# Kernel tuning notes

Hardware: AMD Instinct MI355X
Metric: run time of the kernel (lower is better)

The kernel has to match this reference:

```python
import jax, jax.numpy as jnp
import numpy as np

EPS = 1e-6
NEG = -10000.0
B, T, V, D, H, L, F = 2, 1024, 32000, 1024, 16, 4, 2730
DH = D // H
SCALE = 1.0 / np.sqrt(DH)


def alibi_slopes(n_head):
    # standard ALiBi geometric slopes (n_head is a power of 2 here)
    start = 2.0 ** (-8.0 / n_head)
    return jnp.asarray([start ** (i + 1) for i in range(n_head)], dtype=jnp.float32)


def rational_softmax(x, eps=EPS):
    # exp-free softmax: Pade [0/2] rational surrogate of exp on shifted (<=0) scores
    s = x - jnp.max(x, axis=-1, keepdims=True)
    num = 1.0 / (1.0 - s + 0.5 * s * s)
    return num / (jnp.sum(num, axis=-1, keepdims=True) + eps)


def me_norm(x, w, eps=EPS):
    # mean-error norm: x / (mean|x| + eps) * w
    return x / (jnp.mean(jnp.abs(x), axis=-1, keepdims=True) + eps) * w


def setup_inputs() -> dict:
    key = jax.random.key(0)
    ks = jax.random.split(key, 9)
    std = 0.02
    return {
        "input_ids": jax.random.randint(ks[0], (B, T), 0, V),
        "embed_w":   jax.random.normal(ks[1], (V, D), jnp.float32) * std,  # tied with head
        "qkv_w":     jax.random.normal(ks[2], (L, 3 * D, D), jnp.float32) * std,
        "out_w":     jax.random.normal(ks[3], (L, D, D), jnp.float32) * std,
        "gate_w":    jax.random.normal(ks[4], (L, 2 * F, D), jnp.float32) * std,
        "wout_w":    jax.random.normal(ks[5], (L, D, F), jnp.float32) * std,
        "norm1_w":   jnp.ones((L, D), jnp.float32),
        "norm2_w":   jnp.ones((L, D), jnp.float32),
        "normf_w":   jnp.ones((D,), jnp.float32),
    }


def _forward(input_ids, embed_w, qkv_w, out_w, gate_w, wout_w, norm1_w, norm2_w, normf_w):
    slopes = alibi_slopes(H)                       # [H]
    pos = jnp.arange(T)
    rel = jnp.abs(pos[:, None] - pos[None, :]).astype(jnp.float32)  # [T,T]
    alibi = -rel[None] * slopes[:, None, None]     # [H,T,T]
    causal = jnp.triu(jnp.ones((T, T), bool), k=1) # future positions

    x = embed_w[input_ids]                         # [B,T,D]

    def block(x, p):
        w_qkv, w_out, w_gate, w_wout, n1, n2 = p
        h = me_norm(x, n1)
        qkv = (h @ w_qkv.T).reshape(B, T, 3, H, DH).transpose(2, 0, 3, 1, 4)
        q, k, v = qkv[0], qkv[1], qkv[2]           # [B,H,T,DH]
        scores = jnp.einsum('bhtd,bhsd->bhts', q, k) * SCALE + alibi
        scores = jnp.where(causal[None, None], NEG, scores)
        probs = rational_softmax(scores)
        o = jnp.einsum('bhts,bhsd->bhtd', probs, v)
        o = o.transpose(0, 2, 1, 3).reshape(B, T, D)
        x = x + o @ w_out.T
        h = me_norm(x, n2)
        gv = h @ w_gate.T                           # [B,T,2F]
        gate, val = gv[..., :F], gv[..., F:]
        sigma = 0.5 * (gate / (jnp.abs(gate) + 1.0) + 1.0)  # rational sigmoid
        x = x + (gate * sigma * val) @ w_wout.T
        return x, None

    x, _ = jax.lax.scan(block, x, (qkv_w, out_w, gate_w, wout_w, norm1_w, norm2_w))
    x = me_norm(x, normf_w)
    logits = x @ embed_w.T                          # tied head, [B,T,V]
    return logits


def reference(input_ids, embed_w, qkv_w, out_w, gate_w, wout_w, norm1_w, norm2_w, normf_w):
    return _forward(input_ids, embed_w, qkv_w, out_w, gate_w, wout_w, norm1_w, norm2_w, normf_w)
```

## Files before the change

kernel.cpp:

```cpp
#include <hip/hip_runtime.h>
#include <math.h>

typedef __attribute__((ext_vector_type(8))) short bf16x8;
typedef __attribute__((ext_vector_type(4))) float f32x4;

namespace {
constexpr int Bc = 2, Tc = 1024, Dc = 1024, Hc = 16, Fc = 2730;
constexpr int Fp = 2752;
constexpr int Gp = 5504;
constexpr int Mc = Bc * Tc;
constexpr float EPSc = 1e-6f;
constexpr float NEGc = -10000.0f;
constexpr float SCALEc = 0.125f;
}

__device__ __forceinline__ unsigned short f2b(float f) {
    unsigned int u = __float_as_uint(f);
    u += 0x7FFFu + ((u >> 16) & 1u);
    return (unsigned short)(u >> 16);
}

__global__ void k_embed(const int* __restrict__ ids, const float* __restrict__ ew,
                        float* __restrict__ x) {
    int row = blockIdx.x;
    int id = ids[row];
    const float4* src = (const float4*)(ew + (size_t)id * Dc);
    float4* dst = (float4*)(x + (size_t)row * Dc);
    dst[threadIdx.x] = src[threadIdx.x];
}

__global__ void k_conv(const float* __restrict__ in, unsigned short* __restrict__ out) {
    size_t i = ((size_t)blockIdx.x * 256 + threadIdx.x) * 4;
    float4 v = *(const float4*)(in + i);
    ushort4 o;
    o.x = f2b(v.x); o.y = f2b(v.y); o.z = f2b(v.z); o.w = f2b(v.w);
    *(ushort4*)(out + i) = o;
}

__global__ void k_conv_gate_ilv(const float* __restrict__ in, unsigned short* __restrict__ out) {
    int r = blockIdx.x;
    int c = threadIdx.x * 4;
    ushort4 o;
    if (r < 2 * Fc) {
        int src = (r >> 1) + (r & 1) * Fc;
        float4 v = *(const float4*)(in + (size_t)src * Dc + c);
        o.x = f2b(v.x); o.y = f2b(v.y); o.z = f2b(v.z); o.w = f2b(v.w);
    } else {
        o.x = o.y = o.z = o.w = 0;
    }
    *(ushort4*)(out + (size_t)r * Dc + c) = o;
}

__global__ void k_conv_padk(const float* __restrict__ in, unsigned short* __restrict__ out) {
    int r = blockIdx.x;
    for (int c = threadIdx.x; c < Fp; c += 256) {
        float v = (c < Fc) ? in[(size_t)r * Fc + c] : 0.0f;
        out[(size_t)r * Fp + c] = f2b(v);
    }
}

__global__ void k_menorm_b(const float* __restrict__ x, const float* __restrict__ w,
                           unsigned short* __restrict__ out) {
    int row = blockIdx.x;
    float4 v = ((const float4*)(x + (size_t)row * Dc))[threadIdx.x];
    float s = fabsf(v.x) + fabsf(v.y) + fabsf(v.z) + fabsf(v.w);
#pragma unroll
    for (int m = 32; m >= 1; m >>= 1) s += __shfl_xor(s, m);
    __shared__ float ws4[4];
    if ((threadIdx.x & 63) == 0) ws4[threadIdx.x >> 6] = s;
    __syncthreads();
    float tot = ws4[0] + ws4[1] + ws4[2] + ws4[3];
    float inv = 1.0f / (tot / (float)Dc + EPSc);
    float4 wv = ((const float4*)w)[threadIdx.x];
    ushort4 o;
    o.x = f2b(v.x * inv * wv.x);
    o.y = f2b(v.y * inv * wv.y);
    o.z = f2b(v.z * inv * wv.z);
    o.w = f2b(v.w * inv * wv.w);
    ((ushort4*)(out + (size_t)row * Dc))[threadIdx.x] = o;
}

template <int MODE, int BM>
__global__ __launch_bounds__(256) void k_mfma_gemm(
    const unsigned short* __restrict__ A, const unsigned short* __restrict__ Bw,
    const float* __restrict__ Res, float* __restrict__ C,
    unsigned short* __restrict__ U0, unsigned short* __restrict__ U1,
    unsigned short* __restrict__ U2, int N, int K) {
    constexpr int MFR = BM / 32;
    __shared__ __align__(16) unsigned short As[BM * 64];
    __shared__ __align__(16) unsigned short Bs[128 * 64];
    const int tid = threadIdx.x;
    const int lane = tid & 63;
    const int wid = tid >> 6;
    const int wr = wid >> 1, wc = wid & 1;
    const int l15 = lane & 15, g = lane >> 4;

    const int nwg = gridDim.x * gridDim.y;
    int w = blockIdx.y * gridDim.x + blockIdx.x;
    int f = (nwg & 7) ? w : ((w & 7) * (nwg >> 3) + (w >> 3));
    const int bm = (f % gridDim.x) * BM, bn = (f / gridDim.x) * 128;

    f32x4 acc[MFR][4] = {};

    const int nk = K >> 6;
    for (int kt = 0; kt < nk; ++kt) {
        const int k0 = kt << 6;
#pragma unroll
        for (int it = 0; it < MFR; ++it) {
            int ci = it * 256 + tid;
            int r = ci >> 3;
            int sc = (ci & 7) ^ (r & 7);
            __builtin_amdgcn_global_load_lds(
                (const __attribute__((address_space(1))) void*)(A + (size_t)(bm + r) * K + k0 + sc * 8),
                (__attribute__((address_space(3))) void*)(As + ci * 8), 16, 0, 0);
        }
#pragma unroll
        for (int it = 0; it < 4; ++it) {
            int ci = it * 256 + tid;
            int r = ci >> 3;
            int sc = (ci & 7) ^ (r & 7);
            __builtin_amdgcn_global_load_lds(
                (const __attribute__((address_space(1))) void*)(Bw + (size_t)(bn + r) * K + k0 + sc * 8),
                (__attribute__((address_space(3))) void*)(Bs + ci * 8), 16, 0, 0);
        }
        __syncthreads();
#pragma unroll
        for (int kk = 0; kk < 2; ++kk) {
            bf16x8 af[MFR], bfr[4];
            const int kc = kk * 4 + g;
#pragma unroll
            for (int m = 0; m < MFR; ++m) {
                int row = wr * (BM / 2) + m * 16 + l15;
                af[m] = *(const bf16x8*)&As[(row * 8 + (kc ^ (row & 7))) * 8];
            }
#pragma unroll
            for (int n = 0; n < 4; ++n) {
                int col = wc * 64 + n * 16 + l15;
                bfr[n] = *(const bf16x8*)&Bs[(col * 8 + (kc ^ (col & 7))) * 8];
            }
#pragma unroll
            for (int m = 0; m < MFR; ++m)
#pragma unroll
                for (int n = 0; n < 4; ++n)
                    acc[m][n] = __builtin_amdgcn_mfma_f32_16x16x32_bf16(af[m], bfr[n], acc[m][n], 0, 0, 0);
        }
        __syncthreads();
    }

#pragma unroll
    for (int m = 0; m < MFR; ++m) {
        int row0 = bm + wr * (BM / 2) + m * 16 + (g << 2);
#pragma unroll
        for (int n = 0; n < 4; ++n) {
            int col = bn + wc * 64 + n * 16 + l15;
            if constexpr (MODE == 0 || MODE == 1) {
#pragma unroll
                for (int j = 0; j < 4; ++j) {
                    size_t idx = (size_t)(row0 + j) * N + col;
                    float v = acc[m][n][j];
                    if (MODE == 1) v += Res[idx];
                    C[idx] = v;
                }
            } else if constexpr (MODE == 2) {
                if (col < 2048) {
                    unsigned short* dst = (col < 1024) ? U0 : U1;
                    int hh = (col & 1023) >> 6, dh = col & 63;
#pragma unroll
                    for (int j = 0; j < 4; ++j) {
                        int row = row0 + j;
                        int b = row >> 10, t = row & 1023;
                        dst[((size_t)((b * Hc + hh) * Tc + t)) * 64 + dh] = f2b(acc[m][n][j]);
                    }
                } else {
                    int hh = (col >> 6) & 15, dh = col & 63;
                    int b = row0 >> 10, t = row0 & 1023;
                    ushort4 o4;
                    o4.x = f2b(acc[m][n][0]); o4.y = f2b(acc[m][n][1]);
                    o4.z = f2b(acc[m][n][2]); o4.w = f2b(acc[m][n][3]);
                    *(ushort4*)&U2[((size_t)((b * Hc + hh) * 64 + dh)) * Tc + t] = o4;
                }
            } else {
                float pv[4];
#pragma unroll
                for (int j = 0; j < 4; ++j) pv[j] = __shfl_xor(acc[m][n][j], 1);
                if ((l15 & 1) == 0) {
                    int fq = col >> 1;
#pragma unroll
                    for (int j = 0; j < 4; ++j) {
                        float gate = acc[m][n][j], val = pv[j];
                        float sigma = 0.5f * (gate / (fabsf(gate) + 1.0f) + 1.0f);
                        U0[(size_t)(row0 + j) * Fp + fq] = f2b(gate * sigma * val);
                    }
                }
            }
        }
    }
}

__global__ __launch_bounds__(512, 2) void k_gemm_8ph(
    const unsigned short* __restrict__ A, const unsigned short* __restrict__ Bw,
    float* __restrict__ C, int N, int K) {
    __shared__ __align__(16) unsigned short As[2][256 * 64];
    __shared__ __align__(16) unsigned short Bs[2][256 * 64];
    const int tid = threadIdx.x;
    const int lane = tid & 63, wid = tid >> 6;
    const int wm = wid >> 2, wn = wid & 3;
    const int l15 = lane & 15, g = lane >> 4;

    const int nwg = gridDim.x * gridDim.y;
    int w = blockIdx.y * gridDim.x + blockIdx.x;
    int f = (nwg & 7) ? w : ((w & 7) * (nwg >> 3) + (w >> 3));
    const int bm = (f % gridDim.x) * 256;
    const int bn = (f / gridDim.x) * 256;

    const int nk = K >> 6;

    f32x4 acc[8][4] = {};

#define STAGE8(buf, kt)                                                                          \
    {                                                                                            \
        _Pragma("unroll") for (int it = 0; it < 4; ++it) {                                       \
            int ci = it * 512 + tid;                                                             \
            int r = ci >> 3, c = (ci & 7) ^ (r & 7);                                             \
            __builtin_amdgcn_global_load_lds(                                                    \
                (const __attribute__((address_space(1))) void*)(A + (size_t)(bm + r) * K + (kt) * 64 + c * 8), \
                (__attribute__((address_space(3))) void*)(&As[buf][ci * 8]), 16, 0, 0);          \
        }                                                                                        \
        _Pragma("unroll") for (int it = 0; it < 4; ++it) {                                       \
            int ci = it * 512 + tid;                                                             \
            int r = ci >> 3, c = (ci & 7) ^ (r & 7);                                             \
            __builtin_amdgcn_global_load_lds(                                                    \
                (const __attribute__((address_space(1))) void*)(Bw + (size_t)(bn + r) * K + (kt) * 64 + c * 8), \
                (__attribute__((address_space(3))) void*)(&Bs[buf][ci * 8]), 16, 0, 0);          \
        }                                                                                        \
    }

    STAGE8(0, 0);
    STAGE8(1, 1);
    asm volatile("s_waitcnt vmcnt(8)" ::: "memory");
    __builtin_amdgcn_s_barrier();

    for (int kt = 0; kt < nk; ++kt) {
        const int buf = kt & 1;
        const unsigned short* Ab = As[buf];
        const unsigned short* Bb = Bs[buf];
        bf16x8 bfr[4][2];
#pragma unroll
        for (int p = 0; p < 4; ++p) {
            bf16x8 af[2][2];
#pragma unroll
            for (int le = 0; le < 2; ++le) {
                int row = wm * 128 + (p * 2 + le) * 16 + l15;
#pragma unroll
                for (int kk = 0; kk < 2; ++kk) {
                    int kc = kk * 4 + g;
                    af[le][kk] = *(const bf16x8*)&Ab[(row * 8 + (kc ^ (row & 7))) * 8];
                }
            }
            if (p == 0) {
#pragma unroll
                for (int n = 0; n < 4; ++n) {
                    int col = wn * 64 + n * 16 + l15;
#pragma unroll
                    for (int kk = 0; kk < 2; ++kk) {
                        int kc = kk * 4 + g;
                        bfr[n][kk] = *(const bf16x8*)&Bb[(col * 8 + (kc ^ (col & 7))) * 8];
                    }
                }
            }
            __builtin_amdgcn_s_barrier();
            if (p == 3 && kt + 2 < nk) STAGE8(buf, kt + 2);
            __builtin_amdgcn_s_setprio(1);
#pragma unroll
            for (int kk = 0; kk < 2; ++kk)
#pragma unroll
                for (int le = 0; le < 2; ++le)
#pragma unroll
                    for (int n = 0; n < 4; ++n)
                        acc[p * 2 + le][n] = __builtin_amdgcn_mfma_f32_16x16x32_bf16(
                            af[le][kk], bfr[n][kk], acc[p * 2 + le][n], 0, 0, 0);
            __builtin_amdgcn_s_setprio(0);
            if (p == 3) {
                if (kt + 2 < nk) {
                    asm volatile("s_waitcnt vmcnt(8)" ::: "memory");
                } else {
                    asm volatile("s_waitcnt vmcnt(0)" ::: "memory");
                }
            }
            __builtin_amdgcn_s_barrier();
        }
    }
#undef STAGE8

#pragma unroll
    for (int m = 0; m < 8; ++m) {
        int row0 = bm + wm * 128 + m * 16 + (g << 2);
#pragma unroll
        for (int n = 0; n < 4; ++n) {
            int col = bn + wn * 64 + n * 16 + l15;
#pragma unroll
            for (int j = 0; j < 4; ++j)
                C[(size_t)(row0 + j) * N + col] = acc[m][n][j];
        }
    }
}

__global__ __launch_bounds__(256) void k_attn_mfma(
    const unsigned short* __restrict__ Qh, const unsigned short* __restrict__ Kh,
    const unsigned short* __restrict__ Vt, unsigned short* __restrict__ o) {
    const int q0 = blockIdx.x * 64;
    const int h = blockIdx.y, b = blockIdx.z;
    const int bh = b * Hc + h;
    const float slope = exp2f(-0.5f * (float)(h + 1));

    __shared__ __align__(16) unsigned short Ks[64 * 64];
    __shared__ __align__(16) unsigned short Vs[64 * 64];
    __shared__ __align__(16) unsigned short Ps[4][16 * 64];

    const int tid = threadIdx.x, lane = tid & 63, wid = tid >> 6;
    const int q0w = q0 + wid * 16;
    const int l15 = lane & 15, g = lane >> 4;

    const unsigned short* qbase = Qh + ((size_t)(bh * Tc + q0w + l15)) * 64 + g * 8;
    bf16x8 qf[2];
    qf[0] = *(const bf16x8*)qbase;
    qf[1] = *(const bf16x8*)(qbase + 32);

    const int nt = q0 / 64 + 1;

    f32x4 mx = {-3e38f, -3e38f, -3e38f, -3e38f};
    for (int it = 0; it < nt; ++it) {
        const int st = it * 64;
        __syncthreads();
#pragma unroll
        for (int half = 0; half < 2; ++half) {
            int ci = half * 256 + tid;
            int r = ci >> 3, sc = (ci & 7) ^ (r & 7);
            __builtin_amdgcn_global_load_lds(
                (const __attribute__((address_space(1))) void*)(Kh + ((size_t)(bh * Tc + st + r)) * 64 + sc * 8),
                (__attribute__((address_space(3))) void*)(Ks + ci * 8), 16, 0, 0);
        }
        __syncthreads();
#pragma unroll
        for (int si = 0; si < 4; ++si) {
            f32x4 d = {0.f, 0.f, 0.f, 0.f};
#pragma unroll
            for (int kc = 0; kc < 2; ++kc) {
                int r2 = si * 16 + l15;
                int c2 = kc * 4 + g;
                bf16x8 bk = *(const bf16x8*)&Ks[(r2 * 8 + (c2 ^ (r2 & 7))) * 8];
                d = __builtin_amdgcn_mfma_f32_16x16x32_bf16(qf[kc], bk, d, 0, 0, 0);
            }
            int s = st + si * 16 + l15;
#pragma unroll
            for (int j = 0; j < 4; ++j) {
                int t = q0w + g * 4 + j;
                float scv = (s <= t) ? d[j] * SCALEc - slope * (float)(t - s) : -3e38f;
                mx[j] = fmaxf(mx[j], scv);
            }
        }
    }
#pragma unroll
    for (int m = 8; m >= 1; m >>= 1)
#pragma unroll
        for (int j = 0; j < 4; ++j) mx[j] = fmaxf(mx[j], __shfl_xor(mx[j], m));

    f32x4 sum = {0.f, 0.f, 0.f, 0.f};
    f32x4 oacc[4] = {};
    for (int it = 0; it < nt; ++it) {
        const int st = it * 64;
        __syncthreads();
#pragma unroll
        for (int half = 0; half < 2; ++half) {
            int ci = half * 256 + tid;
            int r = ci >> 3, sc = (ci & 7) ^ (r & 7);
            __builtin_amdgcn_global_load_lds(
                (const __attribute__((address_space(1))) void*)(Kh + ((size_t)(bh * Tc + st + r)) * 64 + sc * 8),
                (__attribute__((address_space(3))) void*)(Ks + ci * 8), 16, 0, 0);
            __builtin_amdgcn_global_load_lds(
                (const __attribute__((address_space(1))) void*)(Vt + ((size_t)(bh * 64 + r)) * Tc + st + sc * 8),
                (__attribute__((address_space(3))) void*)(Vs + ci * 8), 16, 0, 0);
        }
        __syncthreads();
#pragma unroll
        for (int si = 0; si < 4; ++si) {
            f32x4 d = {0.f, 0.f, 0.f, 0.f};
#pragma unroll
            for (int kc = 0; kc < 2; ++kc) {
                int r2 = si * 16 + l15;
                int c2 = kc * 4 + g;
                bf16x8 bk = *(const bf16x8*)&Ks[(r2 * 8 + (c2 ^ (r2 & 7))) * 8];
                d = __builtin_amdgcn_mfma_f32_16x16x32_bf16(qf[kc], bk, d, 0, 0, 0);
            }
            int sl = si * 16 + l15;
            int s = st + sl;
            int chunk = sl >> 3, coff = sl & 7;
#pragma unroll
            for (int j = 0; j < 4; ++j) {
                int t = q0w + g * 4 + j;
                int q = g * 4 + j;
                unsigned short pb = 0;
                if (s <= t) {
                    float sv = d[j] * SCALEc - slope * (float)(t - s) - mx[j];
                    float num = __builtin_amdgcn_rcpf(fmaf(0.5f * sv, sv, 1.0f - sv));
                    sum[j] += num;
                    pb = f2b(num);
                }
                Ps[wid][q * 64 + ((chunk ^ (q & 7)) * 8) + coff] = pb;
            }
        }
        __syncthreads();
#pragma unroll
        for (int kc = 0; kc < 2; ++kc) {
            int c2 = kc * 4 + g;
            bf16x8 pa = *(const bf16x8*)&Ps[wid][(l15 * 8 + (c2 ^ (l15 & 7))) * 8];
#pragma unroll
            for (int n = 0; n < 4; ++n) {
                int r2 = n * 16 + l15;
                bf16x8 vb = *(const bf16x8*)&Vs[(r2 * 8 + (c2 ^ (r2 & 7))) * 8];
                oacc[n] = __builtin_amdgcn_mfma_f32_16x16x32_bf16(pa, vb, oacc[n], 0, 0, 0);
            }
        }
    }
#pragma unroll
    for (int m = 8; m >= 1; m >>= 1)
#pragma unroll
        for (int j = 0; j < 4; ++j) sum[j] += __shfl_xor(sum[j], m);

#pragma unroll
    for (int j = 0; j < 4; ++j) {
        int t = q0w + g * 4 + j;
        float svm = NEGc - mx[j];
        float mnum = __builtin_amdgcn_rcpf(fmaf(0.5f * svm, svm, 1.0f - svm));
        float inv = __builtin_amdgcn_rcpf(sum[j] + (float)(Tc - 1 - t) * mnum + EPSc);
#pragma unroll
        for (int n = 0; n < 4; ++n) {
            o[((size_t)(b * Tc + t)) * Dc + h * 64 + n * 16 + l15] = f2b(oacc[n][j] * inv);
        }
    }
}

extern "C" void kernel_launch(void* const* d_in, const int* in_sizes, int n_in,
                              void* d_out, int out_size, void* d_ws, size_t ws_size,
                              hipStream_t stream) {
    const int* ids = (const int*)d_in[0];
    const float* embed_w = (const float*)d_in[1];
    const float* qkv_w = (const float*)d_in[2];
    const float* out_w = (const float*)d_in[3];
    const float* gate_w = (const float*)d_in[4];
    const float* wout_w = (const float*)d_in[5];
    const float* n1 = (const float*)d_in[6];
    const float* n2 = (const float*)d_in[7];
    const float* nf = (const float*)d_in[8];
    float* outp = (float*)d_out;

    char* ws = (char*)d_ws;
    float* x = (float*)(ws + 0);
    unsigned short* h = (unsigned short*)(ws + 8388608);
    unsigned short* Qh = (unsigned short*)(ws + 12582912);
    unsigned short* Kh = (unsigned short*)(ws + 16777216);
    unsigned short* Vt = (unsigned short*)(ws + 20971520);
    unsigned short* g = (unsigned short*)(ws + 25165824);
    unsigned short* w1 = (unsigned short*)(ws + 36438016);
    unsigned short* wo_b = (unsigned short*)(ws + 42729472);
    unsigned short* wg_b = (unsigned short*)(ws + 44826624);
    unsigned short* emb_b = (unsigned short*)(ws + 12582912);

    dim3 blk(256);

    k_embed<<<dim3(Mc), blk, 0, stream>>>(ids, embed_w, x);

    for (int l = 0; l < 4; l++) {
        const float* wq = qkv_w + (size_t)l * 3 * Dc * Dc;
        const float* wo = out_w + (size_t)l * Dc * Dc;
        const float* wg = gate_w + (size_t)l * 2 * Fc * Dc;
        const float* ww = wout_w + (size_t)l * Dc * Fc;

        k_conv<<<dim3(3072), blk, 0, stream>>>(wq, w1);
        k_conv<<<dim3(1024), blk, 0, stream>>>(wo, wo_b);
        k_conv_gate_ilv<<<dim3(Gp), blk, 0, stream>>>(wg, wg_b);

        k_menorm_b<<<dim3(Mc), blk, 0, stream>>>(x, n1 + (size_t)l * Dc, h);
        k_mfma_gemm<2, 128><<<dim3(16, 24), blk, 0, stream>>>(h, w1, nullptr, nullptr, Qh, Kh, Vt, 3 * Dc, Dc);
        k_conv_padk<<<dim3(1024), blk, 0, stream>>>(ww, w1);
        k_attn_mfma<<<dim3(Tc / 64, Hc, Bc), blk, 0, stream>>>(Qh, Kh, Vt, h);
        k_mfma_gemm<1, 64><<<dim3(32, 8), blk, 0, stream>>>(h, wo_b, x, x, nullptr, nullptr, nullptr, Dc, Dc);
        k_menorm_b<<<dim3(Mc), blk, 0, stream>>>(x, n2 + (size_t)l * Dc, h);
        k_mfma_gemm<3, 128><<<dim3(16, Gp / 128), blk, 0, stream>>>(h, wg_b, nullptr, nullptr, g, nullptr, nullptr, Gp, Dc);
        k_mfma_gemm<1, 64><<<dim3(32, 8), blk, 0, stream>>>(g, w1, x, x, nullptr, nullptr, nullptr, Dc, Fp);
    }

    k_menorm_b<<<dim3(Mc), blk, 0, stream>>>(x, nf, h);
    k_conv<<<dim3(32000), blk, 0, stream>>>(embed_w, emb_b);
    k_gemm_8ph<<<dim3(8, 125), dim3(512), 0, stream>>>(h, emb_b, outp, 32000, Dc);
}
```

Baseline: 1.027 ms.

## Load A operand directly from global into registers, keep only B in LDS

The 8-phase GEMM no longer stages the A tile through LDS. Each wave now loads its A fragments straight from global memory into registers, double-buffered one phase ahead. B is still staged through LDS with async global-to-LDS loads, and the barriers are reduced to one __syncthreads per k-tile. This halves LDS use and removes the A LDS reads and write waits. In exchange, the four waves sharing the same A rows each fetch them separately, and the row-strided loads are less coalesced, which adds cache and global traffic. The explicit vmcnt waits are gone, so correctness now depends on the compiler's implicit waits at __syncthreads.

```diff
diff --git a/kernel.cpp b/kernel.cpp
--- a/kernel.cpp
+++ b/kernel.cpp
@@ -200,7 +200,6 @@
 __global__ __launch_bounds__(512, 2) void k_gemm_8ph(
     const unsigned short* __restrict__ A, const unsigned short* __restrict__ Bw,
     float* __restrict__ C, int N, int K) {
-    __shared__ __align__(16) unsigned short As[2][256 * 64];
     __shared__ __align__(16) unsigned short Bs[2][256 * 64];
     const int tid = threadIdx.x;
     const int lane = tid & 63, wid = tid >> 6;
@@ -214,62 +213,63 @@
     const int bn = (f / gridDim.x) * 256;
 
     const int nk = K >> 6;
-
     f32x4 acc[8][4] = {};
 
-#define STAGE8(buf, kt)                                                                          \
-    {                                                                                            \
-        _Pragma("unroll") for (int it = 0; it < 4; ++it) {                                       \
-            int ci = it * 512 + tid;                                                             \
-            int r = ci >> 3, c = (ci & 7) ^ (r & 7);                                             \
-            __builtin_amdgcn_global_load_lds(                                                    \
-                (const __attribute__((address_space(1))) void*)(A + (size_t)(bm + r) * K + (kt) * 64 + c * 8), \
-                (__attribute__((address_space(3))) void*)(&As[buf][ci * 8]), 16, 0, 0);          \
-        }                                                                                        \
-        _Pragma("unroll") for (int it = 0; it < 4; ++it) {                                       \
-            int ci = it * 512 + tid;                                                             \
-            int r = ci >> 3, c = (ci & 7) ^ (r & 7);                                             \
-            __builtin_amdgcn_global_load_lds(                                                    \
+    const unsigned short* pA = A + (size_t)(bm + wm * 128 + l15) * K + g * 8;
+
+#define STAGE_B(buf, kt)                                                                          \
+    {                                                                                             \
+        _Pragma("unroll") for (int it = 0; it < 4; ++it) {                                        \
+            int ci = it * 512 + tid;                                                              \
+            int r = ci >> 3, c = (ci & 7) ^ (r & 7);                                              \
+            __builtin_amdgcn_global_load_lds(                                                     \
                 (const __attribute__((address_space(1))) void*)(Bw + (size_t)(bn + r) * K + (kt) * 64 + c * 8), \
-                (__attribute__((address_space(3))) void*)(&Bs[buf][ci * 8]), 16, 0, 0);          \
-        }                                                                                        \
-    }
-
-    STAGE8(0, 0);
-    STAGE8(1, 1);
-    asm volatile("s_waitcnt vmcnt(8)" ::: "memory");
-    __builtin_amdgcn_s_barrier();
+                (__attribute__((address_space(3))) void*)(&Bs[buf][ci * 8]), 16, 0, 0);           \
+        }                                                                                         \
+    }
+
+    STAGE_B(0, 0);
+    STAGE_B(1, 1);
+
+    bf16x8 af[2][2][2];
+#pragma unroll
+    for (int le = 0; le < 2; ++le)
+#pragma unroll
+        for (int kk = 0; kk < 2; ++kk)
+            af[0][le][kk] = *(const bf16x8*)(pA + (size_t)le * 16 * K + kk * 32);
+
+    __syncthreads();
 
     for (int kt = 0; kt < nk; ++kt) {
         const int buf = kt & 1;
-        const unsigned short* Ab = As[buf];
         const unsigned short* Bb = Bs[buf];
         bf16x8 bfr[4][2];
 #pragma unroll
+        for (int n = 0; n < 4; ++n) {
+            int col = wn * 64 + n * 16 + l15;
+#pragma unroll
+            for (int kk = 0; kk < 2; ++kk) {
+                int kc = kk * 4 + g;
+                bfr[n][kk] = *(const bf16x8*)&Bb[(col * 8 + (kc ^ (col & 7))) * 8];
+            }
+        }
+        __syncthreads();
+        if (kt + 2 < nk) STAGE_B(buf, kt + 2);
+
+        const unsigned short* pAk = pA + (size_t)kt * 64;
+#pragma unroll
         for (int p = 0; p < 4; ++p) {
-            bf16x8 af[2][2];
-#pragma unroll
-            for (int le = 0; le < 2; ++le) {
-                int row = wm * 128 + (p * 2 + le) * 16 + l15;
-#pragma unroll
-                for (int kk = 0; kk < 2; ++kk) {
-                    int kc = kk * 4 + g;
-                    af[le][kk] = *(const bf16x8*)&Ab[(row * 8 + (kc ^ (row & 7))) * 8];
-                }
-            }
-            if (p == 0) {
-#pragma unroll
-                for (int n = 0; n < 4; ++n) {
-                    int col = wn * 64 + n * 16 + l15;
-#pragma unroll
-                    for (int kk = 0; kk < 2; ++kk) {
-                        int kc = kk * 4 + g;
-                        bfr[n][kk] = *(const bf16x8*)&Bb[(col * 8 + (kc ^ (col & 7))) * 8];
-                    }
-                }
-            }
-            __builtin_amdgcn_s_barrier();
-            if (p == 3 && kt + 2 < nk) STAGE8(buf, kt + 2);
+            if (p < 3 || kt + 1 < nk) {
+                const unsigned short* src = (p < 3)
+                    ? (pAk + (size_t)(p + 1) * 32 * K)
+                    : (pAk + 64);
+#pragma unroll
+                for (int le = 0; le < 2; ++le)
+#pragma unroll
+                    for (int kk = 0; kk < 2; ++kk)
+                        af[(p + 1) & 1][le][kk] =
+                            *(const bf16x8*)(src + (size_t)le * 16 * K + kk * 32);
+            }
             __builtin_amdgcn_s_setprio(1);
 #pragma unroll
             for (int kk = 0; kk < 2; ++kk)
@@ -278,19 +278,11 @@
 #pragma unroll
                     for (int n = 0; n < 4; ++n)
                         acc[p * 2 + le][n] = __builtin_amdgcn_mfma_f32_16x16x32_bf16(
-                            af[le][kk], bfr[n][kk], acc[p * 2 + le][n], 0, 0, 0);
+                            af[p & 1][le][kk], bfr[n][kk], acc[p * 2 + le][n], 0, 0, 0);
             __builtin_amdgcn_s_setprio(0);
-            if (p == 3) {
-                if (kt + 2 < nk) {
-                    asm volatile("s_waitcnt vmcnt(8)" ::: "memory");
-                } else {
-                    asm volatile("s_waitcnt vmcnt(0)" ::: "memory");
-                }
-            }
-            __builtin_amdgcn_s_barrier();
-        }
-    }
-#undef STAGE8
+        }
+    }
+#undef STAGE_B
 
 #pragma unroll
     for (int m = 0; m < 8; ++m) {
```

Result: slower. 1.132 ms (+10.2%).

## Double-buffer K/V tiles in attention and skip causal masking on full tiles

Applied to the files above, without the earlier changes.

The attention kernel now keeps two LDS buffers for K and V. It prefetches the next tile with global_load_lds while the current tile is computed, and uses one waitcnt plus barrier per iteration instead of two __syncthreads around each load. Tiles that lie entirely below the diagonal skip the per-element causal comparison. The cost is twice the LDS for K and V, which may lower occupancy. The barrier between the per-wave P write and the P read is also dropped, which relies on LDS ops within a wave completing in order.

```diff
diff --git a/kernel.cpp b/kernel.cpp
--- a/kernel.cpp
+++ b/kernel.cpp
@@ -308,13 +308,14 @@
 __global__ __launch_bounds__(256) void k_attn_mfma(
     const unsigned short* __restrict__ Qh, const unsigned short* __restrict__ Kh,
     const unsigned short* __restrict__ Vt, unsigned short* __restrict__ o) {
-    const int q0 = blockIdx.x * 64;
+    const int bx = blockIdx.x;
+    const int q0 = bx * 64;
     const int h = blockIdx.y, b = blockIdx.z;
     const int bh = b * Hc + h;
     const float slope = exp2f(-0.5f * (float)(h + 1));
 
-    __shared__ __align__(16) unsigned short Ks[64 * 64];
-    __shared__ __align__(16) unsigned short Vs[64 * 64];
+    __shared__ __align__(16) unsigned short Ks[2][64 * 64];
+    __shared__ __align__(16) unsigned short Vs[2][64 * 64];
     __shared__ __align__(16) unsigned short Ps[4][16 * 64];
 
     const int tid = threadIdx.x, lane = tid & 63, wid = tid >> 6;
@@ -326,39 +327,59 @@
     qf[0] = *(const bf16x8*)qbase;
     qf[1] = *(const bf16x8*)(qbase + 32);
 
-    const int nt = q0 / 64 + 1;
+    const int nt = bx + 1;
+
+#define STAGE_K(buf, it)                                                                         \
+    {                                                                                            \
+        _Pragma("unroll") for (int half = 0; half < 2; ++half) {                                 \
+            int ci = half * 256 + tid;                                                           \
+            int r = ci >> 3, sc = (ci & 7) ^ (r & 7);                                            \
+            __builtin_amdgcn_global_load_lds(                                                    \
+                (const __attribute__((address_space(1))) void*)(Kh + ((size_t)(bh * Tc + (it) * 64 + r)) * 64 + sc * 8), \
+                (__attribute__((address_space(3))) void*)(&Ks[buf][ci * 8]), 16, 0, 0);          \
+        }                                                                                        \
+    }
+#define STAGE_V(buf, it)                                                                         \
+    {                                                                                            \
+        _Pragma("unroll") for (int half = 0; half < 2; ++half) {                                 \
+            int ci = half * 256 + tid;                                                           \
+            int r = ci >> 3, sc = (ci & 7) ^ (r & 7);                                            \
+            __builtin_amdgcn_global_load_lds(                                                    \
+                (const __attribute__((address_space(1))) void*)(Vt + ((size_t)(bh * 64 + r)) * Tc + (it) * 64 + sc * 8), \
+                (__attribute__((address_space(3))) void*)(&Vs[buf][ci * 8]), 16, 0, 0);          \
+        }                                                                                        \
+    }
 
     f32x4 mx = {-3e38f, -3e38f, -3e38f, -3e38f};
+    STAGE_K(0, 0);
+    asm volatile("s_waitcnt vmcnt(0)" ::: "memory");
+    __builtin_amdgcn_s_barrier();
     for (int it = 0; it < nt; ++it) {
+        const int buf = it & 1;
+        if (it + 1 < nt) STAGE_K(buf ^ 1, it + 1);
         const int st = it * 64;
-        __syncthreads();
-#pragma unroll
-        for (int half = 0; half < 2; ++half) {
-            int ci = half * 256 + tid;
-            int r = ci >> 3, sc = (ci & 7) ^ (r & 7);
-            __builtin_amdgcn_global_load_lds(
-                (const __attribute__((address_space(1))) void*)(Kh + ((size_t)(bh * Tc + st + r)) * 64 + sc * 8),
-                (__attribute__((address_space(3))) void*)(Ks + ci * 8), 16, 0, 0);
-        }
-        __syncthreads();
+        const bool fullTile = (it < bx);
 #pragma unroll
         for (int si = 0; si < 4; ++si) {
             f32x4 d = {0.f, 0.f, 0.f, 0.f};
 #pragma unroll
-            for (int kc = 0; kc < 2; ++kc) {
+            for (int kc2 = 0; kc2 < 2; ++kc2) {
                 int r2 = si * 16 + l15;
-                int c2 = kc * 4 + g;
-                bf16x8 bk = *(const bf16x8*)&Ks[(r2 * 8 + (c2 ^ (r2 & 7))) * 8];
-                d = __builtin_amdgcn_mfma_f32_16x16x32_bf16(qf[kc], bk, d, 0, 0, 0);
+                int c2 = kc2 * 4 + g;
+                bf16x8 bk = *(const bf16x8*)&Ks[buf][(r2 * 8 + (c2 ^ (r2 & 7))) * 8];
+                d = __builtin_amdgcn_mfma_f32_16x16x32_bf16(qf[kc2], bk, d, 0, 0, 0);
             }
             int s = st + si * 16 + l15;
 #pragma unroll
             for (int j = 0; j < 4; ++j) {
                 int t = q0w + g * 4 + j;
-                float scv = (s <= t) ? d[j] * SCALEc - slope * (float)(t - s) : -3e38f;
+                float scv = d[j] * SCALEc - slope * (float)(t - s);
+                if (!fullTile && s > t) scv = -3e38f;
                 mx[j] = fmaxf(mx[j], scv);
             }
         }
+        asm volatile("s_waitcnt vmcnt(0)" ::: "memory");
+        __builtin_amdgcn_s_barrier();
     }
 #pragma unroll
     for (int m = 8; m >= 1; m >>= 1)
@@ -367,30 +388,24 @@
 
     f32x4 sum = {0.f, 0.f, 0.f, 0.f};
     f32x4 oacc[4] = {};
+    STAGE_K(0, 0);
+    STAGE_V(0, 0);
+    asm volatile("s_waitcnt vmcnt(0)" ::: "memory");
+    __builtin_amdgcn_s_barrier();
     for (int it = 0; it < nt; ++it) {
+        const int buf = it & 1;
+        if (it + 1 < nt) { STAGE_K(buf ^ 1, it + 1); STAGE_V(buf ^ 1, it + 1); }
         const int st = it * 64;
-        __syncthreads();
-#pragma unroll
-        for (int half = 0; half < 2; ++half) {
-            int ci = half * 256 + tid;
-            int r = ci >> 3, sc = (ci & 7) ^ (r & 7);
-            __builtin_amdgcn_global_load_lds(
-                (const __attribute__((address_space(1))) void*)(Kh + ((size_t)(bh * Tc + st + r)) * 64 + sc * 8),
-                (__attribute__((address_space(3))) void*)(Ks + ci * 8), 16, 0, 0);
-            __builtin_amdgcn_global_load_lds(
-                (const __attribute__((address_space(1))) void*)(Vt + ((size_t)(bh * 64 + r)) * Tc + st + sc * 8),
-                (__attribute__((address_space(3))) void*)(Vs + ci * 8), 16, 0, 0);
-        }
-        __syncthreads();
+        const bool fullTile = (it < bx);
 #pragma unroll
         for (int si = 0; si < 4; ++si) {
             f32x4 d = {0.f, 0.f, 0.f, 0.f};
 #pragma unroll
-            for (int kc = 0; kc < 2; ++kc) {
+            for (int kc2 = 0; kc2 < 2; ++kc2) {
                 int r2 = si * 16 + l15;
-                int c2 = kc * 4 + g;
-                bf16x8 bk = *(const bf16x8*)&Ks[(r2 * 8 + (c2 ^ (r2 & 7))) * 8];
-                d = __builtin_amdgcn_mfma_f32_16x16x32_bf16(qf[kc], bk, d, 0, 0, 0);
+                int c2 = kc2 * 4 + g;
+                bf16x8 bk = *(const bf16x8*)&Ks[buf][(r2 * 8 + (c2 ^ (r2 & 7))) * 8];
+                d = __builtin_amdgcn_mfma_f32_16x16x32_bf16(qf[kc2], bk, d, 0, 0, 0);
             }
             int sl = si * 16 + l15;
             int s = st + sl;
@@ -400,7 +415,7 @@
                 int t = q0w + g * 4 + j;
                 int q = g * 4 + j;
                 unsigned short pb = 0;
-                if (s <= t) {
+                if (fullTile || s <= t) {
                     float sv = d[j] * SCALEc - slope * (float)(t - s) - mx[j];
                     float num = __builtin_amdgcn_rcpf(fmaf(0.5f * sv, sv, 1.0f - sv));
                     sum[j] += num;
@@ -409,19 +424,22 @@
                 Ps[wid][q * 64 + ((chunk ^ (q & 7)) * 8) + coff] = pb;
             }
         }
-        __syncthreads();
-#pragma unroll
-        for (int kc = 0; kc < 2; ++kc) {
-            int c2 = kc * 4 + g;
+#pragma unroll
+        for (int kc2 = 0; kc2 < 2; ++kc2) {
+            int c2 = kc2 * 4 + g;
             bf16x8 pa = *(const bf16x8*)&Ps[wid][(l15 * 8 + (c2 ^ (l15 & 7))) * 8];
 #pragma unroll
             for (int n = 0; n < 4; ++n) {
                 int r2 = n * 16 + l15;
-                bf16x8 vb = *(const bf16x8*)&Vs[(r2 * 8 + (c2 ^ (r2 & 7))) * 8];
+                bf16x8 vb = *(const bf16x8*)&Vs[buf][(r2 * 8 + (c2 ^ (r2 & 7))) * 8];
                 oacc[n] = __builtin_amdgcn_mfma_f32_16x16x32_bf16(pa, vb, oacc[n], 0, 0, 0);
             }
         }
-    }
+        asm volatile("s_waitcnt vmcnt(0)" ::: "memory");
+        __builtin_amdgcn_s_barrier();
+    }
+#undef STAGE_K
+#undef STAGE_V
 #pragma unroll
     for (int m = 8; m >= 1; m >>= 1)
 #pragma unroll
```

Measured after the change: 1.045 ms. About the same (+1.8%).
